# Kernel tuning notes

Measured on AMD Instinct MI355X. Metric: run time of the kernel, lower is better.

## Reference

```python
import jax, jax.numpy as jnp
import numpy as np

MUL = 512
IR_DIMS = (1, 3, 5)          # 0e, 1e, 2e -> 2l+1
PW = MUL ** -0.5             # path_weight = (mul_in * n_paths_to_out)^-0.5, n_paths=1 each


def setup_inputs() -> dict:
    key = jax.random.key(0)
    k_x, k0, k1, k2 = jax.random.split(key, 4)
    B = 4096
    D = MUL * sum(IR_DIMS)  # 4608
    return {
        "x": jax.random.normal(k_x, (B, D), dtype=jnp.float32),
        "w0": jax.random.normal(k0, (MUL, MUL), dtype=jnp.float32),
        "w1": jax.random.normal(k1, (MUL, MUL), dtype=jnp.float32),
        "w2": jax.random.normal(k2, (MUL, MUL), dtype=jnp.float32),
        "b0": jnp.zeros((MUL,), dtype=jnp.float32),  # bias only on scalar 0e irrep
    }


def reference(x, w0, w1, w2, b0):
    B = x.shape[0]
    # split x into per-irrep blocks (B, mul, 2l+1), as Irreps.as_list does
    offs = np.cumsum([0] + [MUL * d for d in IR_DIMS])
    blocks = [x[:, offs[i]:offs[i + 1]].reshape(B, MUL, IR_DIMS[i]) for i in range(3)]
    outs = []
    for blk, w, d in zip(blocks, (w0, w1, w2), IR_DIMS):
        # path_weight * einsum('uw,bui->bwi'), then flatten to mul_ir_out.dim
        o = PW * jnp.einsum('uw,bui->bwi', w, blk)
        outs.append(o.reshape(B, MUL * d))
    # bias instruction: path_weight 1.0, only on the scalar (0e) output irrep
    outs[0] = outs[0] + b0[None, :]
    return jnp.concatenate(outs, axis=-1)
```

## Files before the change

kernel.cpp:

```cpp
#include <hip/hip_runtime.h>


#define BATCH 4096
#define DTOT 4608
#define NMUL 512

typedef __attribute__((ext_vector_type(8))) short short8;
typedef __attribute__((ext_vector_type(8))) unsigned short ushort8;
typedef __attribute__((ext_vector_type(4))) float float4v;

#define XPL_BYTES (9ull * BATCH * NMUL * 2)

__device__ __forceinline__ unsigned short f2bf(float f) {
    unsigned int u = __builtin_bit_cast(unsigned int, f);
    return (unsigned short)((u + 0x7fffu + ((u >> 16) & 1u)) >> 16);
}
__device__ __forceinline__ void gld16(const unsigned short* g, unsigned short* l) {
    __builtin_amdgcn_global_load_lds(
        (const __attribute__((address_space(1))) unsigned int*)(const void*)g,
        (__attribute__((address_space(3))) unsigned int*)(void*)l, 16, 0, 0);
}
__device__ __forceinline__ void waitvm0() {
    asm volatile("s_waitcnt vmcnt(0)" ::: "memory");
}
__device__ __forceinline__ void waitlgkm0() {
    asm volatile("s_waitcnt lgkmcnt(0)" ::: "memory");
}
__device__ __forceinline__ void colmap(int col, int& c, int& u) {
    if (col < 512)       { c = 0; u = col; }
    else if (col < 2048) { int t = col - 512;  c = 1 + t % 3; u = t / 3; }
    else                 { int t = col - 2048; c = 4 + t % 5; u = t / 5; }
}

__global__ __launch_bounds__(256) void prep(const float* __restrict__ x,
                                            const float* __restrict__ w0,
                                            const float* __restrict__ w1,
                                            const float* __restrict__ w2,
                                            unsigned short* __restrict__ Xp,
                                            unsigned short* __restrict__ Wt) {
    __shared__ unsigned short buf[4608];
    const int tid = threadIdx.x;
    const int b = blockIdx.x;
    if (b < BATCH) {
        const int row = b;
        const float4v* src = (const float4v*)(x + (size_t)row * DTOT);
        for (int p = tid; p < DTOT / 4; p += 256) {
            float4v v = src[p];
#pragma unroll
            for (int j = 0; j < 4; ++j) {
                int c, u; colmap(p * 4 + j, c, u);
                buf[c * NMUL + u] = f2bf(v[j]);
            }
        }
        __syncthreads();
        for (int q = tid; q < DTOT / 8; q += 256) {
            const int c = q >> 6, u8 = q & 63;
            *(ushort8*)(Xp + ((size_t)(c * BATCH + row) * NMUL) + u8 * 8) =
                *(const ushort8*)&buf[c * NMUL + u8 * 8];
        }
    } else {
        const int t = b - BATCH;
        const int ch = t >> 6, tt = t & 63;
        const int tk = (tt >> 3) * 64, tn = (tt & 7) * 64;
        const float* W = (ch == 0) ? w0 : (ch == 1) ? w1 : w2;
        const int r0 = tid >> 4, c4 = (tid & 15) * 4;
#pragma unroll
        for (int rr = 0; rr < 4; ++rr) {
            const int row = r0 + rr * 16;
            float4v v = *(const float4v*)(W + (size_t)(tk + row) * NMUL + tn + c4);
#pragma unroll
            for (int j = 0; j < 4; ++j) buf[(c4 + j) * 72 + row] = f2bf(v[j]);
        }
        __syncthreads();
        for (int q = tid; q < 512; q += 256) {
            const int nn = q >> 3, k8 = q & 7;
            *(ushort8*)(Wt + ((size_t)(ch * NMUL + tn + nn) * NMUL) + tk + k8 * 8) =
                *(const ushort8*)&buf[nn * 72 + k8 * 8];
        }
    }
}

template <int D, int PBASE, int XOFF, int WCH>
__device__ __forceinline__ void body_d35(int rel,
                                         const unsigned short* __restrict__ Xp,
                                         const unsigned short* __restrict__ Wt,
                                         float* __restrict__ out,
                                         unsigned short* As,
                                         unsigned short* Bs) {
    const int tid = threadIdx.x;
    const int lane = tid & 63;
    const int w = tid >> 6;
    const int lr = lane & 15;
    const int lq = lane >> 4;

    const int n0 = (rel & 7) * 64;
    const int m0 = (rel >> 3) * 64;

    const int ksw = ((lane & 3) ^ ((lane >> 3) & 3)) * 8;
    const int rsw = (lq ^ ((lr >> 1) & 3)) * 8;

    const unsigned short* Ag =
        Xp + ((size_t)(PBASE + w) * BATCH + m0 + (lane >> 2)) * NMUL + ksw;
    const unsigned short* Bg =
        Wt + ((size_t)WCH * NMUL + n0 + (lane >> 2)) * NMUL + ksw;
    unsigned short* Al = As + w * 2048;

    float4v acc[4][4];
#pragma unroll
    for (int a = 0; a < 4; ++a)
#pragma unroll
        for (int b = 0; b < 4; ++b) acc[a][b] = (float4v)0.f;

    for (int kt = 0; kt < 16; ++kt) {
        const int ko = kt * 32;
        if (w < D) {
#pragma unroll
            for (int p = 0; p < 4; ++p)
                gld16(Ag + (size_t)p * 16 * NMUL + ko, Al + p * 512);
        }
        if (w < 4)
            gld16(Bg + (size_t)w * 16 * NMUL + ko, Bs + w * 512);
        waitvm0();
        __builtin_amdgcn_s_barrier();
        if (w < D) {
            const unsigned short* Bl = Bs;
            short8 af[4], bf[4];
#pragma unroll
            for (int mi = 0; mi < 4; ++mi)
                af[mi] = *(const short8*)(Al + (mi * 16 + lr) * 32 + rsw);
#pragma unroll
            for (int ni = 0; ni < 4; ++ni)
                bf[ni] = *(const short8*)(Bl + (ni * 16 + lr) * 32 + rsw);
            __builtin_amdgcn_s_setprio(1);
#pragma unroll
            for (int mi = 0; mi < 4; ++mi)
#pragma unroll
                for (int ni = 0; ni < 4; ++ni)
                    acc[mi][ni] = __builtin_amdgcn_mfma_f32_16x16x32_bf16(
                        af[mi], bf[ni], acc[mi][ni], 0, 0, 0);
            __builtin_amdgcn_s_setprio(0);
        }
        waitlgkm0();
        __builtin_amdgcn_s_barrier();
    }

    float* Cs = (float*)As;
    const float PW = 0.044194173824159216f;
#pragma unroll
    for (int mc = 0; mc < 4; ++mc) {
        if (w < D) {
#pragma unroll
            for (int ni = 0; ni < 4; ++ni)
#pragma unroll
                for (int r = 0; r < 4; ++r)
                    Cs[(lq * 4 + r) * (64 * D) + (ni * 16 + lr) * D + w] =
                        acc[mc][ni][r] * PW;
        }
        __syncthreads();
        constexpr int F4 = 16 * 16 * D;
        for (int f = tid; f < F4; f += 320) {
            const int row = f / (16 * D);
            const int c4  = f % (16 * D);
            *(float4v*)(out + (size_t)(m0 + mc * 16 + row) * DTOT + XOFF + n0 * D + c4 * 4) =
                *(const float4v*)(Cs + f * 4);
        }
        __syncthreads();
    }
}

__device__ __forceinline__ void body_d1(int rel,
                                        const unsigned short* __restrict__ Xp,
                                        const unsigned short* __restrict__ Wt,
                                        const float* __restrict__ b0,
                                        float* __restrict__ out,
                                        unsigned short* As) {
    const int tid = threadIdx.x;
    const int lane = tid & 63;
    const int w = tid >> 6;
    const int lr = lane & 15;
    const int lq = lane >> 4;
    const int wm = (w >> 1) * 64;
    const int wn = (w & 1) * 64;

    const int n0 = (rel & 3) * 128;
    const int m0 = (rel >> 2) * 128;

    const int ksw = ((lane & 3) ^ ((lane >> 3) & 3)) * 8;
    const int rsw = (lq ^ ((lr >> 1) & 3)) * 8;

    const unsigned short* Ag = Xp + (size_t)(m0 + w * 32 + (lane >> 2)) * NMUL + ksw;
    const unsigned short* Bg = Wt + (size_t)(n0 + w * 32 + (lane >> 2)) * NMUL + ksw;
    unsigned short* Al = As + w * 1024;
    unsigned short* Bl = As + 4096 + w * 1024;

    float4v acc[4][4];
#pragma unroll
    for (int a = 0; a < 4; ++a)
#pragma unroll
        for (int b = 0; b < 4; ++b) acc[a][b] = (float4v)0.f;

    for (int kt = 0; kt < 16; ++kt) {
        const int ko = kt * 32;
        if (w < 4) {
            gld16(Ag + ko, Al);
            gld16(Ag + ko + 16 * NMUL, Al + 512);
            gld16(Bg + ko, Bl);
            gld16(Bg + ko + 16 * NMUL, Bl + 512);
        }
        waitvm0();
        __builtin_amdgcn_s_barrier();
        if (w < 4) {
            const unsigned short* Ab = As;
            const unsigned short* Bb = As + 4096;
            short8 af[4], bf[4];
#pragma unroll
            for (int mi = 0; mi < 4; ++mi)
                af[mi] = *(const short8*)(Ab + (wm + mi * 16 + lr) * 32 + rsw);
#pragma unroll
            for (int ni = 0; ni < 4; ++ni)
                bf[ni] = *(const short8*)(Bb + (wn + ni * 16 + lr) * 32 + rsw);
            __builtin_amdgcn_s_setprio(1);
#pragma unroll
            for (int mi = 0; mi < 4; ++mi)
#pragma unroll
                for (int ni = 0; ni < 4; ++ni)
                    acc[mi][ni] = __builtin_amdgcn_mfma_f32_16x16x32_bf16(
                        af[mi], bf[ni], acc[mi][ni], 0, 0, 0);
            __builtin_amdgcn_s_setprio(0);
        }
        waitlgkm0();
        __builtin_amdgcn_s_barrier();
    }

    if (w < 4) {
        const float PW = 0.044194173824159216f;
#pragma unroll
        for (int ni = 0; ni < 4; ++ni) {
            const int col = n0 + wn + ni * 16 + lr;
            const float bias = b0[col];
#pragma unroll
            for (int mi = 0; mi < 4; ++mi)
#pragma unroll
                for (int r = 0; r < 4; ++r)
                    out[(size_t)(m0 + wm + mi * 16 + lq * 4 + r) * DTOT + col] =
                        acc[mi][ni][r] * PW + bias;
        }
    }
}

__global__ __launch_bounds__(320) void gemm_all(const unsigned short* __restrict__ Xp,
                                                const unsigned short* __restrict__ Wt,
                                                const float* __restrict__ b0,
                                                float* __restrict__ out) {
    __shared__ __align__(16) unsigned short As[10240];
    __shared__ __align__(16) unsigned short Bs[2048];

    const int hw = blockIdx.x;
    const int xcd = hw & 7, j = hw >> 3;
    const int b = ((xcd + ((j >> 3) << 3)) << 3) + (j & 7);

    if (b < 512)       body_d35<5, 4, 2048, 2>(b, Xp, Wt, out, As, Bs);
    else if (b < 1024) body_d35<3, 1, 512, 1>(b - 512, Xp, Wt, out, As, Bs);
    else               body_d1(b - 1024, Xp, Wt, b0, out, As);
}

extern "C" void kernel_launch(void* const* d_in, const int* in_sizes, int n_in,
                              void* d_out, int out_size, void* d_ws, size_t ws_size,
                              hipStream_t stream) {
    const float* x  = (const float*)d_in[0];
    const float* w0 = (const float*)d_in[1];
    const float* w1 = (const float*)d_in[2];
    const float* w2 = (const float*)d_in[3];
    const float* b0 = (const float*)d_in[4];
    float* out = (float*)d_out;

    unsigned short* Xp = (unsigned short*)d_ws;
    unsigned short* Wt = (unsigned short*)((char*)d_ws + XPL_BYTES);

    prep<<<dim3(BATCH + 192), dim3(256), 0, stream>>>(x, w0, w1, w2, Xp, Wt);
    gemm_all<<<dim3(1152), dim3(320), 0, stream>>>(Xp, Wt, b0, out);
}
```

Before: 180.2 us.

## Triple-buffer LDS tiles with prefetch depth two in GEMM loops

Replaces the single-buffered load/wait/compute loop with a three-slot LDS ring. Global-to-LDS loads are issued two k-steps ahead, and each wave waits only for its oldest outstanding loads using per-wave vmcnt counts. This removes one barrier per iteration and lets memory latency overlap MFMA work. LDS use per block grows from 24KB to 72KB, which may cut occupancy, and the hand-tuned vmcnt values are fragile if the load counts change.

```diff
diff --git a/kernel.cpp b/kernel.cpp
--- a/kernel.cpp
+++ b/kernel.cpp
@@ -4,6 +4,7 @@
 #define BATCH 4096
 #define DTOT 4608
 #define NMUL 512
+#define BSTRIDE 12288
 
 typedef __attribute__((ext_vector_type(8))) short short8;
 typedef __attribute__((ext_vector_type(8))) unsigned short ushort8;
@@ -20,11 +21,9 @@
         (const __attribute__((address_space(1))) unsigned int*)(const void*)g,
         (__attribute__((address_space(3))) unsigned int*)(void*)l, 16, 0, 0);
 }
-__device__ __forceinline__ void waitvm0() {
-    asm volatile("s_waitcnt vmcnt(0)" ::: "memory");
-}
-__device__ __forceinline__ void waitlgkm0() {
-    asm volatile("s_waitcnt lgkmcnt(0)" ::: "memory");
+template <int N>
+__device__ __forceinline__ void waitvm() {
+    asm volatile("s_waitcnt vmcnt(%0)" :: "n"(N) : "memory");
 }
 __device__ __forceinline__ void colmap(int col, int& c, int& u) {
     if (col < 512)       { c = 0; u = col; }
@@ -85,8 +84,7 @@
                                          const unsigned short* __restrict__ Xp,
                                          const unsigned short* __restrict__ Wt,
                                          float* __restrict__ out,
-                                         unsigned short* As,
-                                         unsigned short* Bs) {
+                                         unsigned short* LDS) {
     const int tid = threadIdx.x;
     const int lane = tid & 63;
     const int w = tid >> 6;
@@ -103,7 +101,6 @@
         Xp + ((size_t)(PBASE + w) * BATCH + m0 + (lane >> 2)) * NMUL + ksw;
     const unsigned short* Bg =
         Wt + ((size_t)WCH * NMUL + n0 + (lane >> 2)) * NMUL + ksw;
-    unsigned short* Al = As + w * 2048;
 
     float4v acc[4][4];
 #pragma unroll
@@ -111,19 +108,29 @@
 #pragma unroll
         for (int b = 0; b < 4; ++b) acc[a][b] = (float4v)0.f;
 
+    auto stage = [&](int ko, int bo) {
+        if (w < D) {
+#pragma unroll
+            for (int p = 0; p < 4; ++p)
+                gld16(Ag + (size_t)p * 16 * NMUL + ko, LDS + bo + w * 2048 + p * 512);
+        }
+        if (w < 4)
+            gld16(Bg + (size_t)w * 16 * NMUL + ko, LDS + bo + 10240 + w * 512);
+    };
+
+    stage(0, 0);
+    stage(32, BSTRIDE);
+
+    int co = 0, po = 2 * BSTRIDE;
     for (int kt = 0; kt < 16; ++kt) {
-        const int ko = kt * 32;
+        if (kt == 15) { waitvm<0>(); }
+        else if (D == 5) { if (w < 4) waitvm<5>(); else waitvm<4>(); }
+        else             { if (w < 3) waitvm<5>(); else if (w == 3) waitvm<1>(); }
+        __builtin_amdgcn_s_barrier();
+        if (kt < 14) stage((kt + 2) * 32, po);
         if (w < D) {
-#pragma unroll
-            for (int p = 0; p < 4; ++p)
-                gld16(Ag + (size_t)p * 16 * NMUL + ko, Al + p * 512);
-        }
-        if (w < 4)
-            gld16(Bg + (size_t)w * 16 * NMUL + ko, Bs + w * 512);
-        waitvm0();
-        __builtin_amdgcn_s_barrier();
-        if (w < D) {
-            const unsigned short* Bl = Bs;
+            const unsigned short* Al = LDS + co + w * 2048;
+            const unsigned short* Bl = LDS + co + 10240;
             short8 af[4], bf[4];
 #pragma unroll
             for (int mi = 0; mi < 4; ++mi)
@@ -140,12 +147,13 @@
                         af[mi], bf[ni], acc[mi][ni], 0, 0, 0);
             __builtin_amdgcn_s_setprio(0);
         }
-        waitlgkm0();
-        __builtin_amdgcn_s_barrier();
-    }
-
-    float* Cs = (float*)As;
+        co += BSTRIDE; if (co == 3 * BSTRIDE) co = 0;
+        po += BSTRIDE; if (po == 3 * BSTRIDE) po = 0;
+    }
+
+    float* Cs = (float*)LDS;
     const float PW = 0.044194173824159216f;
+    __syncthreads();
 #pragma unroll
     for (int mc = 0; mc < 4; ++mc) {
         if (w < D) {
@@ -173,7 +181,7 @@
                                         const unsigned short* __restrict__ Wt,
                                         const float* __restrict__ b0,
                                         float* __restrict__ out,
-                                        unsigned short* As) {
+                                        unsigned short* LDS) {
     const int tid = threadIdx.x;
     const int lane = tid & 63;
     const int w = tid >> 6;
@@ -190,8 +198,6 @@
 
     const unsigned short* Ag = Xp + (size_t)(m0 + w * 32 + (lane >> 2)) * NMUL + ksw;
     const unsigned short* Bg = Wt + (size_t)(n0 + w * 32 + (lane >> 2)) * NMUL + ksw;
-    unsigned short* Al = As + w * 1024;
-    unsigned short* Bl = As + 4096 + w * 1024;
 
     float4v acc[4][4];
 #pragma unroll
@@ -199,19 +205,27 @@
 #pragma unroll
         for (int b = 0; b < 4; ++b) acc[a][b] = (float4v)0.f;
 
+    auto stage = [&](int ko, int bo) {
+        if (w < 4) {
+            gld16(Ag + ko, LDS + bo + w * 1024);
+            gld16(Ag + ko + 16 * NMUL, LDS + bo + w * 1024 + 512);
+            gld16(Bg + ko, LDS + bo + 4096 + w * 1024);
+            gld16(Bg + ko + 16 * NMUL, LDS + bo + 4096 + w * 1024 + 512);
+        }
+    };
+
+    stage(0, 0);
+    stage(32, BSTRIDE);
+
+    int co = 0, po = 2 * BSTRIDE;
     for (int kt = 0; kt < 16; ++kt) {
-        const int ko = kt * 32;
+        if (kt == 15) { waitvm<0>(); }
+        else if (w < 4) waitvm<4>();
+        __builtin_amdgcn_s_barrier();
+        if (kt < 14) stage((kt + 2) * 32, po);
         if (w < 4) {
-            gld16(Ag + ko, Al);
-            gld16(Ag + ko + 16 * NMUL, Al + 512);
-            gld16(Bg + ko, Bl);
-            gld16(Bg + ko + 16 * NMUL, Bl + 512);
-        }
-        waitvm0();
-        __builtin_amdgcn_s_barrier();
-        if (w < 4) {
-            const unsigned short* Ab = As;
-            const unsigned short* Bb = As + 4096;
+            const unsigned short* Ab = LDS + co;
+            const unsigned short* Bb = LDS + co + 4096;
             short8 af[4], bf[4];
 #pragma unroll
             for (int mi = 0; mi < 4; ++mi)
@@ -228,8 +242,8 @@
                         af[mi], bf[ni], acc[mi][ni], 0, 0, 0);
             __builtin_amdgcn_s_setprio(0);
         }
-        waitlgkm0();
-        __builtin_amdgcn_s_barrier();
+        co += BSTRIDE; if (co == 3 * BSTRIDE) co = 0;
+        po += BSTRIDE; if (po == 3 * BSTRIDE) po = 0;
     }
 
     if (w < 4) {
@@ -252,16 +266,15 @@
                                                 const unsigned short* __restrict__ Wt,
                                                 const float* __restrict__ b0,
                                                 float* __restrict__ out) {
-    __shared__ __align__(16) unsigned short As[10240];
-    __shared__ __align__(16) unsigned short Bs[2048];
+    __shared__ __align__(16) unsigned short LDS[3 * BSTRIDE];
 
     const int hw = blockIdx.x;
     const int xcd = hw & 7, j = hw >> 3;
     const int b = ((xcd + ((j >> 3) << 3)) << 3) + (j & 7);
 
-    if (b < 512)       body_d35<5, 4, 2048, 2>(b, Xp, Wt, out, As, Bs);
-    else if (b < 1024) body_d35<3, 1, 512, 1>(b - 512, Xp, Wt, out, As, Bs);
-    else               body_d1(b - 1024, Xp, Wt, b0, out, As);
+    if (b < 512)       body_d35<5, 4, 2048, 2>(b, Xp, Wt, out, LDS);
+    else if (b < 1024) body_d35<3, 1, 512, 1>(b - 512, Xp, Wt, out, LDS);
+    else               body_d1(b - 1024, Xp, Wt, b0, out, LDS);
 }
 
 extern "C" void kernel_launch(void* const* d_in, const int* in_sizes, int n_in,
```

New measurement: 183.2 us. No clear change (+1.7%).
